# Kernel tuning notes

Hardware: AMD Instinct MI355X
Metric: run time of the kernel (lower is better)

Reference implementation:

```python
import jax, jax.numpy as jnp
from jax import lax
import numpy as np
import math

NUM_CLASSES = 81
N_PER_IMG = 1024
NUM_IMAGES = 8
SCORE_THRESH = 0.05
NMS_THRESH = 0.5
DETS_PER_IMG = 100
WX, WY, WW, WH = 10.0, 10.0, 5.0, 5.0
BBOX_XFORM_CLIP = math.log(1000.0 / 16.0)


def setup_inputs() -> dict:
    key = jax.random.key(0)
    k1, k2, k3, k4 = jax.random.split(key, 4)
    M = NUM_IMAGES * N_PER_IMG
    H, W = 800, 1333
    class_logits = jax.random.normal(k1, (M, NUM_CLASSES), dtype=jnp.float32) * 3.0
    box_regression = jax.random.normal(k2, (M, 4 * NUM_CLASSES), dtype=jnp.float32) * 0.5
    # valid xyxy proposals inside the image
    xy1 = jax.random.uniform(k3, (M, 2), dtype=jnp.float32) * jnp.array([W * 0.7, H * 0.7], jnp.float32)
    wh = jax.random.uniform(k4, (M, 2), dtype=jnp.float32) * jnp.array([W * 0.3, H * 0.3], jnp.float32) + 4.0
    proposals = jnp.concatenate([xy1, xy1 + wh], axis=1)
    return {"class_logits": class_logits, "box_regression": box_regression,
            "proposals": proposals, "height": H, "width": W}


def _decode(rel_codes, boxes):
    widths = boxes[:, 2] - boxes[:, 0] + 1.0
    heights = boxes[:, 3] - boxes[:, 1] + 1.0
    ctr_x = boxes[:, 0] + 0.5 * widths
    ctr_y = boxes[:, 1] + 0.5 * heights
    rel = rel_codes.reshape(rel_codes.shape[0], -1, 4)  # [M, C, 4]
    dx = rel[:, :, 0] / WX
    dy = rel[:, :, 1] / WY
    dw = jnp.minimum(rel[:, :, 2] / WW, BBOX_XFORM_CLIP)
    dh = jnp.minimum(rel[:, :, 3] / WH, BBOX_XFORM_CLIP)
    pctr_x = dx * widths[:, None] + ctr_x[:, None]
    pctr_y = dy * heights[:, None] + ctr_y[:, None]
    pw = jnp.exp(dw) * widths[:, None]
    ph = jnp.exp(dh) * heights[:, None]
    return jnp.stack([pctr_x - 0.5 * pw, pctr_y - 0.5 * ph,
                      pctr_x + 0.5 * pw - 1.0, pctr_y + 0.5 * ph - 1.0], axis=-1)


def _clip(boxes, height, width):
    # boxes [..., 4] xyxy, clamp to [0, W-1] x [0, H-1]
    x = jnp.clip(boxes[..., 0::2], 0.0, float(width - 1))
    y = jnp.clip(boxes[..., 1::2], 0.0, float(height - 1))
    return jnp.stack([x[..., 0], y[..., 0], x[..., 1], y[..., 1]], axis=-1)


def _iou_matrix(b):
    x1, y1, x2, y2 = b[:, 0], b[:, 1], b[:, 2], b[:, 3]
    area = (x2 - x1 + 1.0) * (y2 - y1 + 1.0)
    xx1 = jnp.maximum(x1[:, None], x1[None, :])
    yy1 = jnp.maximum(y1[:, None], y1[None, :])
    xx2 = jnp.minimum(x2[:, None], x2[None, :])
    yy2 = jnp.minimum(y2[:, None], y2[None, :])
    inter = jnp.clip(xx2 - xx1 + 1.0, 0.0) * jnp.clip(yy2 - yy1 + 1.0, 0.0)
    return inter / (area[:, None] + area[None, :] - inter)


def _per_class(scores_j, boxes_j):
    # scores_j [N], boxes_j [N,4] -> sorted scores/boxes + greedy-NMS keep mask
    N = scores_j.shape[0]
    valid = scores_j > SCORE_THRESH
    s = jnp.where(valid, scores_j, 0.0)  # softmax scores are > 0
    order = jnp.argsort(-s)
    s_sorted = s[order]
    b_sorted = boxes_j[order]
    valid_sorted = valid[order]
    iou = _iou_matrix(b_sorted)  # [N, N]
    idxs = jnp.arange(N)

    def body(i, keep):
        sup = (iou[i] > NMS_THRESH) & keep[i] & (idxs > i)
        return keep & ~sup

    keep = lax.fori_loop(0, N, body, valid_sorted)
    return s_sorted, b_sorted, keep


def _per_image(prob_i, boxes_i):
    # prob_i [N, C], boxes_i [N, C, 4]; skip background class 0
    C = prob_i.shape[1]
    fg_scores = prob_i[:, 1:].T                      # [C-1, N]
    fg_boxes = jnp.swapaxes(boxes_i[:, 1:, :], 0, 1)  # [C-1, N, 4]
    s_sorted, b_sorted, keep = jax.vmap(_per_class)(fg_scores, fg_boxes)
    labels = jnp.broadcast_to(jnp.arange(1, C, dtype=jnp.int32)[:, None], s_sorted.shape)
    flat_s = jnp.where(keep, s_sorted, 0.0).reshape(-1)
    vals, idx = lax.top_k(flat_s, DETS_PER_IMG)      # detections-per-image limit
    boxes_out = b_sorted.reshape(-1, 4)[idx]
    labels_out = labels.reshape(-1)[idx]
    ok = vals > SCORE_THRESH
    return (jnp.where(ok, vals, 0.0),
            jnp.where(ok[:, None], boxes_out, 0.0),
            jnp.where(ok, labels_out, 0))


def reference(class_logits, box_regression, proposals, height, width):
    prob = jax.nn.softmax(class_logits, axis=-1)          # [M, C]
    dec = _decode(box_regression, proposals)              # [M, C, 4]
    dec = _clip(dec, height, width)
    B, N, C = NUM_IMAGES, N_PER_IMG, NUM_CLASSES
    prob = prob.reshape(B, N, C)
    dec = dec.reshape(B, N, C, 4)
    scores, boxes, labels = lax.map(lambda a: _per_image(a[0], a[1]), (prob, dec))
    return scores, boxes, labels
```

## Files before the change

### kernel.cpp

```cpp
#include <hip/hip_runtime.h>
#include <stdint.h>
#include <math.h>

#define NCLS 81
#define NFG  80
#define NPI  1024
#define NIMG 8
#define DETS 100
#define SCORE_T 0.05f
#define NMS_T   0.5f
#define NCAND   (NFG * DETS)
#define CAND_CAP 1024
#define FASTN 256
#define ROWS 64

static constexpr float BBOX_CLIP = 4.1351665567423557f;

__global__ __launch_bounds__(256) void softmax_probT(
    const float* __restrict__ logits, float* __restrict__ probT, int M)
{
    __shared__ float tile[ROWS * NCLS];
    __shared__ float mx[ROWS], dn[ROWS];
    int t = threadIdx.x;
    int rbase = blockIdx.x * ROWS;
    for (int idx = t; idx < ROWS * NCLS; idx += 256)
        tile[idx] = logits[(size_t)rbase * NCLS + idx];
    __syncthreads();
    if (t < ROWS) {
        const float* r = tile + t * NCLS;
        float m = r[0];
        #pragma unroll
        for (int j = 1; j < NCLS; ++j) m = fmaxf(m, r[j]);
        float s = 0.f;
        #pragma unroll
        for (int j = 0; j < NCLS; ++j) s += expf(r[j] - m);
        mx[t] = m; dn[t] = s;
    }
    __syncthreads();
    for (int o = t; o < ROWS * NFG; o += 256) {
        int r = o & 63;
        int c = o >> 6;
        probT[(size_t)c * M + rbase + r] = expf(tile[r * NCLS + (c + 1)] - mx[r]) / dn[r];
    }
}

struct ShP2 {
    float box[NPI][4];
    unsigned long long key[NPI];
    unsigned long long skey[NPI];
    int keep[NPI];
    float sbox[FASTN][4];
    float sarea[FASTN];
    unsigned long long mask[FASTN][FASTN/64];
    unsigned long long keepw[FASTN/64];
    unsigned wpre[4];
};

__global__ __launch_bounds__(256) void per_class_nms(
    const float* __restrict__ probT, const float* __restrict__ boxreg,
    const float* __restrict__ props, const int* __restrict__ hptr,
    const int* __restrict__ wptr, int* __restrict__ out_cnt,
    float* __restrict__ out_score, unsigned* __restrict__ out_key,
    float* __restrict__ out_box, int M)
{
    int pid = blockIdx.x;
    int img = pid / NFG;
    int c   = pid % NFG;
    int cls = c + 1;

    __shared__ ShP2 sp;
    __shared__ int cnt;
    int t = threadIdx.x;
    float W1 = (float)(*wptr - 1);
    float H1 = (float)(*hptr - 1);

    if (t == 0) cnt = 0;
    __syncthreads();

    {
        const float4 pv = *(const float4*)(probT + (size_t)c * M + img * NPI + 4 * t);
        float pr[4] = {pv.x, pv.y, pv.z, pv.w};
        #pragma unroll
        for (int j = 0; j < 4; ++j) {
            if (pr[j] > SCORE_T) {
                int m = 4 * t + j;
                int g = img * NPI + m;
                const float4 pb = *(const float4*)(props + (size_t)g * 4);
                float x1 = pb.x, y1 = pb.y, x2 = pb.z, y2 = pb.w;
                float w  = x2 - x1 + 1.0f, h = y2 - y1 + 1.0f;
                float cx = x1 + 0.5f * w,  cy = y1 + 0.5f * h;
                const float4 rc = *(const float4*)(boxreg + (size_t)g * (4 * NCLS) + 4 * cls);
                float dx = rc.x / 10.0f, dy = rc.y / 10.0f;
                float dw = fminf(rc.z / 5.0f, BBOX_CLIP);
                float dh = fminf(rc.w / 5.0f, BBOX_CLIP);
                float pcx = dx * w + cx, pcy = dy * h + cy;
                float pw = expf(dw) * w, ph = expf(dh) * h;
                float bx1 = fminf(fmaxf(pcx - 0.5f * pw, 0.f), W1);
                float by1 = fminf(fmaxf(pcy - 0.5f * ph, 0.f), H1);
                float bx2 = fminf(fmaxf(pcx + 0.5f * pw - 1.0f, 0.f), W1);
                float by2 = fminf(fmaxf(pcy + 0.5f * ph - 1.0f, 0.f), H1);
                sp.box[m][0] = bx1; sp.box[m][1] = by1;
                sp.box[m][2] = bx2; sp.box[m][3] = by2;
                int p = atomicAdd(&cnt, 1);
                sp.key[p] = ((unsigned long long)__float_as_uint(pr[j]) << 32)
                          | (unsigned)(NPI - 1 - m);
            }
        }
    }
    __syncthreads();
    int n = cnt;

    if (n <= 64) {
        if (t < 64) {
            int lane = t;
            unsigned long long k = (lane < n) ? sp.key[lane] : 0ULL;
            #pragma unroll
            for (int kk = 2; kk <= 64; kk <<= 1) {
                #pragma unroll
                for (int j = kk >> 1; j > 0; j >>= 1) {
                    unsigned long long o = __shfl_xor(k, j, 64);
                    bool take_max = (((lane & kk) == 0) == ((lane & j) == 0));
                    k = take_max ? (k > o ? k : o) : (k < o ? k : o);
                }
            }
            bool valid = (lane < n);
            float bx1 = 0.f, by1 = 0.f, bx2 = 0.f, by2 = 0.f, area = 0.f;
            if (valid) {
                int mi = NPI - 1 - (int)(k & 0xFFFFFFFFu);
                bx1 = sp.box[mi][0]; by1 = sp.box[mi][1];
                bx2 = sp.box[mi][2]; by2 = sp.box[mi][3];
                area = (bx2 - bx1 + 1.f) * (by2 - by1 + 1.f);
            }
            unsigned long long sup = 0ULL;
            for (int i = 0; i < n; ++i) {
                bool alive = !((sup >> i) & 1ULL);
                float ax1 = __shfl(bx1, i, 64), ay1 = __shfl(by1, i, 64);
                float ax2 = __shfl(bx2, i, 64), ay2 = __shfl(by2, i, 64);
                float aarea = __shfl(area, i, 64);
                bool s = false;
                if (alive && valid && lane > i) {
                    float xx1 = fmaxf(ax1, bx1), yy1 = fmaxf(ay1, by1);
                    float xx2 = fminf(ax2, bx2), yy2 = fminf(ay2, by2);
                    float iw = fmaxf(xx2 - xx1 + 1.f, 0.f);
                    float ih = fmaxf(yy2 - yy1 + 1.f, 0.f);
                    float inter = iw * ih;
                    s = inter / (aarea + area - inter) > NMS_T;
                }
                sup |= __ballot(s);
            }
            bool kept = valid && !((sup >> lane) & 1ULL);
            unsigned long long keptm = __ballot(kept);
            int rank = __popcll(keptm & ((1ULL << lane) - 1ULL));
            if (kept && rank < DETS) {
                int slot = pid * DETS + rank;
                out_score[slot] = __uint_as_float((unsigned)(k >> 32));
                out_key[slot] = (unsigned)(c * NPI + lane);
                out_box[slot * 4 + 0] = bx1; out_box[slot * 4 + 1] = by1;
                out_box[slot * 4 + 2] = bx2; out_box[slot * 4 + 3] = by2;
            }
            if (lane == 0) {
                int tot = __popcll(keptm);
                out_cnt[pid] = tot < DETS ? tot : DETS;
            }
        }
        return;
    }

    for (int i = t; i < NPI; i += 256) sp.keep[i] = 0;
    for (int i = t; i < n; i += 256) {
        unsigned long long ki = sp.key[i];
        int r = 0;
        for (int j = 0; j < n; ++j) r += (sp.key[j] > ki) ? 1 : 0;
        sp.skey[r] = ki;
    }
    __syncthreads();

    if (n <= FASTN) {
        for (int i = t; i < n; i += 256) {
            int mi = NPI - 1 - (int)(sp.skey[i] & 0xFFFFFFFFu);
            float bx1 = sp.box[mi][0], by1 = sp.box[mi][1];
            float bx2 = sp.box[mi][2], by2 = sp.box[mi][3];
            sp.sbox[i][0] = bx1; sp.sbox[i][1] = by1;
            sp.sbox[i][2] = bx2; sp.sbox[i][3] = by2;
            sp.sarea[i] = (bx2 - bx1 + 1.f) * (by2 - by1 + 1.f);
        }
        __syncthreads();
        int nwords = ((n + 63) >> 6);
        for (int w = t; w < n * (FASTN/64); w += 256) {
            int i = w >> 2, wb = w & 3;
            if (wb >= nwords || ((wb + 1) << 6) - 1 <= i) { sp.mask[i][wb] = 0ULL; continue; }
            float ax1 = sp.sbox[i][0], ay1 = sp.sbox[i][1];
            float ax2 = sp.sbox[i][2], ay2 = sp.sbox[i][3];
            float aarea = sp.sarea[i];
            unsigned long long bits = 0ULL;
            int jbase = wb << 6;
            #pragma unroll 4
            for (int b = 0; b < 64; ++b) {
                int j = jbase + b;
                if (j < n && j > i) {
                    float bx1 = sp.sbox[j][0], by1 = sp.sbox[j][1];
                    float bx2 = sp.sbox[j][2], by2 = sp.sbox[j][3];
                    float xx1 = fmaxf(ax1, bx1), yy1 = fmaxf(ay1, by1);
                    float xx2 = fminf(ax2, bx2), yy2 = fminf(ay2, by2);
                    float iw = fmaxf(xx2 - xx1 + 1.f, 0.f);
                    float ih = fmaxf(yy2 - yy1 + 1.f, 0.f);
                    float inter = iw * ih;
                    if (inter / (aarea + sp.sarea[j] - inter) > NMS_T) bits |= (1ULL << b);
                }
            }
            sp.mask[i][wb] = bits;
        }
        __syncthreads();
        if (t < 64) {
            int lane = t;
            unsigned long long kb = 0ULL;
            if (lane < 4) {
                int rem = n - (lane << 6);
                if (rem >= 64) kb = ~0ULL;
                else if (rem > 0) kb = (1ULL << rem) - 1ULL;
            }
            unsigned long long rm = 0ULL;
            for (int i = 0; i < n; ++i) {
                unsigned long long rw = __shfl(rm, i >> 6, 64);
                if (!((rw >> (i & 63)) & 1ULL)) {
                    unsigned long long mrow = (lane < 4) ? sp.mask[i][lane] : 0ULL;
                    rm |= mrow;
                }
            }
            if (lane < 4) sp.keepw[lane] = kb & ~rm;
        }
        __syncthreads();
        for (int i = t; i < n; i += 256)
            sp.keep[i] = (int)((sp.keepw[i >> 6] >> (i & 63)) & 1ULL);
        __syncthreads();
    } else {
        for (int i = t; i < n; i += 256) sp.keep[i] = 1;
        __syncthreads();
        for (int i = 0; i < n; ++i) {
            if (sp.keep[i]) {
                unsigned long long ki = sp.skey[i];
                int mi = NPI - 1 - (int)(ki & 0xFFFFFFFFu);
                float ax1 = sp.box[mi][0], ay1 = sp.box[mi][1];
                float ax2 = sp.box[mi][2], ay2 = sp.box[mi][3];
                float aarea = (ax2 - ax1 + 1.f) * (ay2 - ay1 + 1.f);
                for (int jj = i + 1 + t; jj < n; jj += 256) {
                    if (sp.keep[jj]) {
                        int mj = NPI - 1 - (int)(sp.skey[jj] & 0xFFFFFFFFu);
                        float bx1 = sp.box[mj][0], by1 = sp.box[mj][1];
                        float bx2 = sp.box[mj][2], by2 = sp.box[mj][3];
                        float xx1 = fmaxf(ax1, bx1), yy1 = fmaxf(ay1, by1);
                        float xx2 = fminf(ax2, bx2), yy2 = fminf(ay2, by2);
                        float iw = fmaxf(xx2 - xx1 + 1.f, 0.f);
                        float ih = fmaxf(yy2 - yy1 + 1.f, 0.f);
                        float inter = iw * ih;
                        float barea = (bx2 - bx1 + 1.f) * (by2 - by1 + 1.f);
                        if (inter / (aarea + barea - inter) > NMS_T) sp.keep[jj] = 0;
                    }
                }
            }
            __syncthreads();
        }
    }

    {
        int lane = t & 63, w = t >> 6;
        int k0 = sp.keep[4 * t], k1 = sp.keep[4 * t + 1];
        int k2 = sp.keep[4 * t + 2], k3 = sp.keep[4 * t + 3];
        unsigned s = (unsigned)(k0 + k1 + k2 + k3);
        unsigned v = s;
        #pragma unroll
        for (int off = 1; off < 64; off <<= 1) {
            unsigned u = __shfl_up(v, off, 64);
            v += (lane >= off) ? u : 0u;
        }
        if (lane == 63) sp.wpre[w] = v;
        __syncthreads();
        unsigned woff = 0;
        for (int w2 = 0; w2 < w; ++w2) woff += sp.wpre[w2];
        unsigned r = v + woff - s;
        #pragma unroll
        for (int j = 0; j < 4; ++j) {
            int i = 4 * t + j;
            int kv = (j == 0) ? k0 : (j == 1) ? k1 : (j == 2) ? k2 : k3;
            if (kv && r < DETS) {
                unsigned long long ki = sp.skey[i];
                int mi = NPI - 1 - (int)(ki & 0xFFFFFFFFu);
                int slot = pid * DETS + (int)r;
                out_score[slot] = __uint_as_float((unsigned)(ki >> 32));
                out_key[slot] = (unsigned)(c * NPI + i);
                out_box[slot * 4 + 0] = sp.box[mi][0];
                out_box[slot * 4 + 1] = sp.box[mi][1];
                out_box[slot * 4 + 2] = sp.box[mi][2];
                out_box[slot * 4 + 3] = sp.box[mi][3];
            }
            r += (unsigned)kv;
        }
        __syncthreads();
        if (t == 0) {
            unsigned tot = sp.wpre[0] + sp.wpre[1] + sp.wpre[2] + sp.wpre[3];
            out_cnt[pid] = (int)(tot < DETS ? tot : DETS);
        }
    }
}

__device__ __forceinline__ void suffix_select256(
    unsigned* hist, unsigned* wtot, int K, int* outB, unsigned* outAbove)
{
    int t = threadIdx.x, lane = t & 63, w = t >> 6;
    unsigned loc[16]; unsigned ps = 0;
    #pragma unroll
    for (int j = 0; j < 16; ++j) { loc[j] = hist[t * 16 + j]; ps += loc[j]; }
    unsigned v = ps;
    #pragma unroll
    for (int off = 1; off < 64; off <<= 1) {
        unsigned u = __shfl_down(v, off, 64);
        v += (lane + off < 64) ? u : 0u;
    }
    if (lane == 0) wtot[w] = v;
    __syncthreads();
    unsigned woff = 0;
    for (int w2 = w + 1; w2 < 4; ++w2) woff += wtot[w2];
    unsigned base = v + woff - ps;
    unsigned suf = 0;
    #pragma unroll
    for (int j = 15; j >= 0; --j) {
        unsigned A = base + suf;
        if ((int)A < K && (int)(A + loc[j]) >= K) { *outB = t * 16 + j; *outAbove = A; }
        suf += loc[j];
    }
    __syncthreads();
}

__global__ __launch_bounds__(256) void topk_merge(
    const int* __restrict__ cnts, const float* __restrict__ escore,
    const unsigned* __restrict__ ekey, const float* __restrict__ ebox,
    float* __restrict__ out)
{
    int img = blockIdx.x;
    __shared__ unsigned sc[NCAND];
    __shared__ unsigned hist[4096];
    __shared__ unsigned long long cand[CAND_CAP];
    __shared__ int scnts[NFG];
    __shared__ unsigned wtot[4];
    __shared__ int sB1, sB2, sNc;
    __shared__ unsigned sAb1, sAb2;

    int t = threadIdx.x;
    if (t < NFG) scnts[t] = cnts[img * NFG + t];
    if (t == 0) { sB1 = 0; sB2 = 0; sNc = 0; sAb1 = 0; sAb2 = 0; }
    for (int i = t; i < 4096; i += 256) hist[i] = 0;
    __syncthreads();

    for (int p = t; p < NCAND; p += 256) {
        unsigned fb = 0;
        if ((p % DETS) < scnts[p / DETS]) fb = __float_as_uint(escore[img * NCAND + p]);
        sc[p] = fb;
        if (fb) atomicAdd(&hist[fb >> 19], 1u);
    }
    __syncthreads();
    suffix_select256(hist, wtot, DETS, &sB1, &sAb1);
    int B1 = sB1; unsigned ab1 = sAb1;

    for (int i = t; i < 4096; i += 256) hist[i] = 0;
    __syncthreads();
    for (int p = t; p < NCAND; p += 256) {
        unsigned fb = sc[p];
        if (fb && (int)(fb >> 19) == B1) atomicAdd(&hist[(fb >> 7) & 0xFFFu], 1u);
    }
    __syncthreads();
    suffix_select256(hist, wtot, DETS - (int)ab1, &sB2, &sAb2);
    int B2 = sB2;

    for (int p = t; p < NCAND; p += 256) {
        unsigned fb = sc[p];
        if (fb) {
            int d1 = (int)(fb >> 19);
            bool ok = d1 > B1 || (d1 == B1 && (int)((fb >> 7) & 0xFFFu) >= B2);
            if (ok) {
                int pos = atomicAdd(&sNc, 1);
                if (pos < CAND_CAP) {
                    unsigned fk = ekey[img * NCAND + p];
                    cand[pos] = ((unsigned long long)fb << 32)
                              | (((0x1FFFFu - fk) << 13) | (unsigned)p);
                }
            }
        }
    }
    __syncthreads();
    int nc = sNc < CAND_CAP ? sNc : CAND_CAP;

    float* oScore = out;
    float* oBox   = out + NIMG * DETS;
    float* oLab   = out + NIMG * DETS * 5;

    for (int k = t; k < DETS; k += 256) {
        if (k >= nc) {
            int o = img * DETS + k;
            oScore[o] = 0.f;
            oBox[o * 4 + 0] = 0.f; oBox[o * 4 + 1] = 0.f;
            oBox[o * 4 + 2] = 0.f; oBox[o * 4 + 3] = 0.f;
            oLab[o] = 0.f;
        }
    }

    for (int i = t; i < nc; i += 256) {
        unsigned long long ki = cand[i];
        int r = 0;
        for (int j = 0; j < nc; ++j) r += (cand[j] > ki) ? 1 : 0;
        if (r < DETS) {
            float scv = __uint_as_float((unsigned)(ki >> 32));
            unsigned low = (unsigned)(ki & 0xFFFFFFFFu);
            unsigned flatkey = 0x1FFFFu - ((low >> 13) & 0x1FFFFu);
            int p = (int)(low & 0x1FFFu);
            int gp = img * NCAND + p;
            int o = img * DETS + r;
            oScore[o] = scv;
            oBox[o * 4 + 0] = ebox[gp * 4 + 0];
            oBox[o * 4 + 1] = ebox[gp * 4 + 1];
            oBox[o * 4 + 2] = ebox[gp * 4 + 2];
            oBox[o * 4 + 3] = ebox[gp * 4 + 3];
            oLab[o] = (float)((flatkey >> 10) + 1);
        }
    }
}

extern "C" void kernel_launch(void* const* d_in, const int* in_sizes, int n_in,
                              void* d_out, int out_size, void* d_ws, size_t ws_size,
                              hipStream_t stream) {
    const float* logits = (const float*)d_in[0];
    const float* boxreg = (const float*)d_in[1];
    const float* props  = (const float*)d_in[2];
    const int*   hptr   = (const int*)d_in[3];
    const int*   wptr   = (const int*)d_in[4];
    float* out = (float*)d_out;
    int M = in_sizes[0] / NCLS;

    char* ws = (char*)d_ws;
    float*    probT  = (float*)ws;    ws += (size_t)NFG * M * sizeof(float);
    int*      gcnt   = (int*)ws;      ws += (size_t)NIMG * NFG * sizeof(int);
    float*    escore = (float*)ws;    ws += (size_t)NIMG * NCAND * sizeof(float);
    unsigned* ekey   = (unsigned*)ws; ws += (size_t)NIMG * NCAND * sizeof(unsigned);
    float*    ebox   = (float*)ws;    ws += (size_t)NIMG * NCAND * 4 * sizeof(float);

    softmax_probT<<<M / ROWS, 256, 0, stream>>>(logits, probT, M);
    per_class_nms<<<NIMG * NFG, 256, 0, stream>>>(
        probT, boxreg, props, hptr, wptr, gcnt, escore, ekey, ebox, M);
    topk_merge<<<NIMG, 256, 0, stream>>>(gcnt, escore, ekey, ebox, out);
}
```

Before: 66.43 us.

## Rewrite per-class NMS as single-wavefront chunked greedy suppression

The per-class NMS kernel now runs one 64-lane wavefront per (image, class) instead of 256 threads. Candidate compaction uses ballot/popcount in place of shared atomics, and the candidate's compacted position is packed into the sort key. The bitmask matrix and serial fallback paths are replaced by a chunked greedy NMS that broadcasts boxes with readlane and keeps a suppression word per 64-box chunk. This cuts shared-memory footprint and block-level syncs, but the O(n^2) rank sort and per-class work now run on a quarter of the threads, and the number of blocks is unchanged.

```diff
diff --git a/kernel.cpp b/kernel.cpp
--- a/kernel.cpp
+++ b/kernel.cpp
@@ -11,10 +11,17 @@
 #define NMS_T   0.5f
 #define NCAND   (NFG * DETS)
 #define CAND_CAP 1024
-#define FASTN 256
 #define ROWS 64
 
 static constexpr float BBOX_CLIP = 4.1351665567423557f;
+
+__device__ __forceinline__ float rlf(float v, int i) {
+#if __has_builtin(__builtin_amdgcn_readlane)
+    return __uint_as_float((unsigned)__builtin_amdgcn_readlane((int)__float_as_uint(v), i));
+#else
+    return __shfl(v, i, 64);
+#endif
+}
 
 __global__ __launch_bounds__(256) void softmax_probT(
     const float* __restrict__ logits, float* __restrict__ probT, int M)
@@ -44,19 +51,7 @@
     }
 }
 
-struct ShP2 {
-    float box[NPI][4];
-    unsigned long long key[NPI];
-    unsigned long long skey[NPI];
-    int keep[NPI];
-    float sbox[FASTN][4];
-    float sarea[FASTN];
-    unsigned long long mask[FASTN][FASTN/64];
-    unsigned long long keepw[FASTN/64];
-    unsigned wpre[4];
-};
-
-__global__ __launch_bounds__(256) void per_class_nms(
+__global__ __launch_bounds__(64) void per_class_nms(
     const float* __restrict__ probT, const float* __restrict__ boxreg,
     const float* __restrict__ props, const int* __restrict__ hptr,
     const int* __restrict__ wptr, int* __restrict__ out_cnt,
@@ -67,24 +62,31 @@
     int img = pid / NFG;
     int c   = pid % NFG;
     int cls = c + 1;
-
-    __shared__ ShP2 sp;
-    __shared__ int cnt;
-    int t = threadIdx.x;
+    int lane = threadIdx.x;
+
+    __shared__ unsigned long long pkey[NPI];
+    __shared__ unsigned long long skey[NPI];
+    __shared__ float pbox[NPI][4];
+    __shared__ unsigned long long remv[16];
+
     float W1 = (float)(*wptr - 1);
     float H1 = (float)(*hptr - 1);
 
-    if (t == 0) cnt = 0;
-    __syncthreads();
-
-    {
-        const float4 pv = *(const float4*)(probT + (size_t)c * M + img * NPI + 4 * t);
+    int cnt = 0;
+    const float* pT = probT + (size_t)c * M + img * NPI;
+
+    #pragma unroll
+    for (int it = 0; it < NPI / 256; ++it) {
+        float4 pv = *(const float4*)(pT + it * 256 + lane * 4);
         float pr[4] = {pv.x, pv.y, pv.z, pv.w};
         #pragma unroll
         for (int j = 0; j < 4; ++j) {
-            if (pr[j] > SCORE_T) {
-                int m = 4 * t + j;
+            bool pass = pr[j] > SCORE_T;
+            unsigned long long bal = __ballot(pass);
+            if (pass) {
+                int m = it * 256 + lane * 4 + j;
                 int g = img * NPI + m;
+                int mypos = cnt + __popcll(bal & ((1ULL << lane) - 1ULL));
                 const float4 pb = *(const float4*)(props + (size_t)g * 4);
                 float x1 = pb.x, y1 = pb.y, x2 = pb.z, y2 = pb.w;
                 float w  = x2 - x1 + 1.0f, h = y2 - y1 + 1.0f;
@@ -99,207 +101,173 @@
                 float by1 = fminf(fmaxf(pcy - 0.5f * ph, 0.f), H1);
                 float bx2 = fminf(fmaxf(pcx + 0.5f * pw - 1.0f, 0.f), W1);
                 float by2 = fminf(fmaxf(pcy + 0.5f * ph - 1.0f, 0.f), H1);
-                sp.box[m][0] = bx1; sp.box[m][1] = by1;
-                sp.box[m][2] = bx2; sp.box[m][3] = by2;
-                int p = atomicAdd(&cnt, 1);
-                sp.key[p] = ((unsigned long long)__float_as_uint(pr[j]) << 32)
-                          | (unsigned)(NPI - 1 - m);
-            }
-        }
-    }
-    __syncthreads();
+                pbox[mypos][0] = bx1; pbox[mypos][1] = by1;
+                pbox[mypos][2] = bx2; pbox[mypos][3] = by2;
+                pkey[mypos] = ((unsigned long long)__float_as_uint(pr[j]) << 32)
+                            | ((unsigned)(NPI - 1 - m) << 10) | (unsigned)mypos;
+            }
+            cnt += __popcll(bal);
+        }
+    }
     int n = cnt;
+    __syncthreads();
 
     if (n <= 64) {
-        if (t < 64) {
-            int lane = t;
-            unsigned long long k = (lane < n) ? sp.key[lane] : 0ULL;
+        unsigned long long k = (lane < n) ? pkey[lane] : 0ULL;
+        #pragma unroll
+        for (int kk = 2; kk <= 64; kk <<= 1) {
             #pragma unroll
-            for (int kk = 2; kk <= 64; kk <<= 1) {
-                #pragma unroll
-                for (int j = kk >> 1; j > 0; j >>= 1) {
-                    unsigned long long o = __shfl_xor(k, j, 64);
-                    bool take_max = (((lane & kk) == 0) == ((lane & j) == 0));
-                    k = take_max ? (k > o ? k : o) : (k < o ? k : o);
-                }
-            }
-            bool valid = (lane < n);
-            float bx1 = 0.f, by1 = 0.f, bx2 = 0.f, by2 = 0.f, area = 0.f;
-            if (valid) {
-                int mi = NPI - 1 - (int)(k & 0xFFFFFFFFu);
-                bx1 = sp.box[mi][0]; by1 = sp.box[mi][1];
-                bx2 = sp.box[mi][2]; by2 = sp.box[mi][3];
-                area = (bx2 - bx1 + 1.f) * (by2 - by1 + 1.f);
-            }
-            unsigned long long sup = 0ULL;
-            for (int i = 0; i < n; ++i) {
-                bool alive = !((sup >> i) & 1ULL);
-                float ax1 = __shfl(bx1, i, 64), ay1 = __shfl(by1, i, 64);
-                float ax2 = __shfl(bx2, i, 64), ay2 = __shfl(by2, i, 64);
-                float aarea = __shfl(area, i, 64);
+            for (int j = kk >> 1; j > 0; j >>= 1) {
+                unsigned long long o = __shfl_xor(k, j, 64);
+                bool take_max = (((lane & kk) == 0) == ((lane & j) == 0));
+                k = take_max ? (k > o ? k : o) : (k < o ? k : o);
+            }
+        }
+        bool valid = (lane < n);
+        float bx1 = 0.f, by1 = 0.f, bx2 = 0.f, by2 = 0.f, area = 0.f;
+        if (valid) {
+            int pos = (int)(k & 0x3FFu);
+            bx1 = pbox[pos][0]; by1 = pbox[pos][1];
+            bx2 = pbox[pos][2]; by2 = pbox[pos][3];
+            area = (bx2 - bx1 + 1.f) * (by2 - by1 + 1.f);
+        }
+        unsigned long long sup = 0ULL;
+        for (int i = 0; i < n; ++i) {
+            if ((sup >> i) & 1ULL) continue;
+            float ax1 = rlf(bx1, i), ay1 = rlf(by1, i);
+            float ax2 = rlf(bx2, i), ay2 = rlf(by2, i);
+            float aarea = rlf(area, i);
+            bool s = false;
+            if (valid && lane > i) {
+                float xx1 = fmaxf(ax1, bx1), yy1 = fmaxf(ay1, by1);
+                float xx2 = fminf(ax2, bx2), yy2 = fminf(ay2, by2);
+                float iw = fmaxf(xx2 - xx1 + 1.f, 0.f);
+                float ih = fmaxf(yy2 - yy1 + 1.f, 0.f);
+                float inter = iw * ih;
+                s = inter / (aarea + area - inter) > NMS_T;
+            }
+            sup |= __ballot(s);
+        }
+        bool kept = valid && !((sup >> lane) & 1ULL);
+        unsigned long long keptm = __ballot(kept);
+        int rank = __popcll(keptm & ((1ULL << lane) - 1ULL));
+        if (kept && rank < DETS) {
+            int slot = pid * DETS + rank;
+            out_score[slot] = __uint_as_float((unsigned)(k >> 32));
+            out_key[slot] = (unsigned)(c * NPI + lane);
+            out_box[slot * 4 + 0] = bx1; out_box[slot * 4 + 1] = by1;
+            out_box[slot * 4 + 2] = bx2; out_box[slot * 4 + 3] = by2;
+        }
+        if (lane == 0) {
+            int tot = __popcll(keptm);
+            out_cnt[pid] = tot < DETS ? tot : DETS;
+        }
+        return;
+    }
+
+    for (int i = lane; i < n; i += 64) {
+        unsigned long long ki = pkey[i];
+        int r = 0;
+        for (int j = 0; j < n; ++j) r += (pkey[j] > ki) ? 1 : 0;
+        skey[r] = ki;
+    }
+    if (lane < 16) remv[lane] = 0ULL;
+    __syncthreads();
+
+    int nch = (n + 63) >> 6;
+    for (int a = 0; a < nch; ++a) {
+        int ea = a * 64 + lane;
+        bool va = ea < n;
+        float bx1 = 0.f, by1 = 0.f, bx2 = 0.f, by2 = 0.f, area = 0.f;
+        if (va) {
+            int pos = (int)(skey[ea] & 0x3FFu);
+            bx1 = pbox[pos][0]; by1 = pbox[pos][1];
+            bx2 = pbox[pos][2]; by2 = pbox[pos][3];
+            area = (bx2 - bx1 + 1.f) * (by2 - by1 + 1.f);
+        }
+        unsigned long long sup = remv[a];
+        int lim = (n - a * 64 < 64) ? (n - a * 64) : 64;
+        for (int i = 0; i < lim; ++i) {
+            if ((sup >> i) & 1ULL) continue;
+            float ax1 = rlf(bx1, i), ay1 = rlf(by1, i);
+            float ax2 = rlf(bx2, i), ay2 = rlf(by2, i);
+            float aarea = rlf(area, i);
+            bool s = false;
+            if (va && lane > i) {
+                float xx1 = fmaxf(ax1, bx1), yy1 = fmaxf(ay1, by1);
+                float xx2 = fminf(ax2, bx2), yy2 = fminf(ay2, by2);
+                float iw = fmaxf(xx2 - xx1 + 1.f, 0.f);
+                float ih = fmaxf(yy2 - yy1 + 1.f, 0.f);
+                float inter = iw * ih;
+                s = inter / (aarea + area - inter) > NMS_T;
+            }
+            sup |= __ballot(s);
+        }
+        if (lane == 0) remv[a] = sup;
+        for (int b = a + 1; b < nch; ++b) {
+            int eb = b * 64 + lane;
+            bool vb = eb < n;
+            float cx1 = 0.f, cy1 = 0.f, cx2 = 0.f, cy2 = 0.f, carea = 0.f;
+            if (vb) {
+                int pos = (int)(skey[eb] & 0x3FFu);
+                cx1 = pbox[pos][0]; cy1 = pbox[pos][1];
+                cx2 = pbox[pos][2]; cy2 = pbox[pos][3];
+                carea = (cx2 - cx1 + 1.f) * (cy2 - cy1 + 1.f);
+            }
+            unsigned long long supb = 0ULL;
+            for (int i = 0; i < lim; ++i) {
+                if ((sup >> i) & 1ULL) continue;
+                float ax1 = rlf(bx1, i), ay1 = rlf(by1, i);
+                float ax2 = rlf(bx2, i), ay2 = rlf(by2, i);
+                float aarea = rlf(area, i);
                 bool s = false;
-                if (alive && valid && lane > i) {
-                    float xx1 = fmaxf(ax1, bx1), yy1 = fmaxf(ay1, by1);
-                    float xx2 = fminf(ax2, bx2), yy2 = fminf(ay2, by2);
+                if (vb) {
+                    float xx1 = fmaxf(ax1, cx1), yy1 = fmaxf(ay1, cy1);
+                    float xx2 = fminf(ax2, cx2), yy2 = fminf(ay2, cy2);
                     float iw = fmaxf(xx2 - xx1 + 1.f, 0.f);
                     float ih = fmaxf(yy2 - yy1 + 1.f, 0.f);
                     float inter = iw * ih;
-                    s = inter / (aarea + area - inter) > NMS_T;
+                    s = inter / (aarea + carea - inter) > NMS_T;
                 }
-                sup |= __ballot(s);
-            }
-            bool kept = valid && !((sup >> lane) & 1ULL);
-            unsigned long long keptm = __ballot(kept);
-            int rank = __popcll(keptm & ((1ULL << lane) - 1ULL));
-            if (kept && rank < DETS) {
-                int slot = pid * DETS + rank;
-                out_score[slot] = __uint_as_float((unsigned)(k >> 32));
-                out_key[slot] = (unsigned)(c * NPI + lane);
-                out_box[slot * 4 + 0] = bx1; out_box[slot * 4 + 1] = by1;
-                out_box[slot * 4 + 2] = bx2; out_box[slot * 4 + 3] = by2;
-            }
-            if (lane == 0) {
-                int tot = __popcll(keptm);
-                out_cnt[pid] = tot < DETS ? tot : DETS;
-            }
-        }
-        return;
-    }
-
-    for (int i = t; i < NPI; i += 256) sp.keep[i] = 0;
-    for (int i = t; i < n; i += 256) {
-        unsigned long long ki = sp.key[i];
-        int r = 0;
-        for (int j = 0; j < n; ++j) r += (sp.key[j] > ki) ? 1 : 0;
-        sp.skey[r] = ki;
-    }
-    __syncthreads();
-
-    if (n <= FASTN) {
-        for (int i = t; i < n; i += 256) {
-            int mi = NPI - 1 - (int)(sp.skey[i] & 0xFFFFFFFFu);
-            float bx1 = sp.box[mi][0], by1 = sp.box[mi][1];
-            float bx2 = sp.box[mi][2], by2 = sp.box[mi][3];
-            sp.sbox[i][0] = bx1; sp.sbox[i][1] = by1;
-            sp.sbox[i][2] = bx2; sp.sbox[i][3] = by2;
-            sp.sarea[i] = (bx2 - bx1 + 1.f) * (by2 - by1 + 1.f);
+                supb |= __ballot(s);
+            }
+            if (lane == 0) remv[b] |= supb;
+            __syncthreads();
         }
         __syncthreads();
-        int nwords = ((n + 63) >> 6);
-        for (int w = t; w < n * (FASTN/64); w += 256) {
-            int i = w >> 2, wb = w & 3;
-            if (wb >= nwords || ((wb + 1) << 6) - 1 <= i) { sp.mask[i][wb] = 0ULL; continue; }
-            float ax1 = sp.sbox[i][0], ay1 = sp.sbox[i][1];
-            float ax2 = sp.sbox[i][2], ay2 = sp.sbox[i][3];
-            float aarea = sp.sarea[i];
-            unsigned long long bits = 0ULL;
-            int jbase = wb << 6;
-            #pragma unroll 4
-            for (int b = 0; b < 64; ++b) {
-                int j = jbase + b;
-                if (j < n && j > i) {
-                    float bx1 = sp.sbox[j][0], by1 = sp.sbox[j][1];
-                    float bx2 = sp.sbox[j][2], by2 = sp.sbox[j][3];
-                    float xx1 = fmaxf(ax1, bx1), yy1 = fmaxf(ay1, by1);
-                    float xx2 = fminf(ax2, bx2), yy2 = fminf(ay2, by2);
-                    float iw = fmaxf(xx2 - xx1 + 1.f, 0.f);
-                    float ih = fmaxf(yy2 - yy1 + 1.f, 0.f);
-                    float inter = iw * ih;
-                    if (inter / (aarea + sp.sarea[j] - inter) > NMS_T) bits |= (1ULL << b);
-                }
-            }
-            sp.mask[i][wb] = bits;
-        }
-        __syncthreads();
-        if (t < 64) {
-            int lane = t;
-            unsigned long long kb = 0ULL;
-            if (lane < 4) {
-                int rem = n - (lane << 6);
-                if (rem >= 64) kb = ~0ULL;
-                else if (rem > 0) kb = (1ULL << rem) - 1ULL;
-            }
-            unsigned long long rm = 0ULL;
-            for (int i = 0; i < n; ++i) {
-                unsigned long long rw = __shfl(rm, i >> 6, 64);
-                if (!((rw >> (i & 63)) & 1ULL)) {
-                    unsigned long long mrow = (lane < 4) ? sp.mask[i][lane] : 0ULL;
-                    rm |= mrow;
-                }
-            }
-            if (lane < 4) sp.keepw[lane] = kb & ~rm;
-        }
-        __syncthreads();
-        for (int i = t; i < n; i += 256)
-            sp.keep[i] = (int)((sp.keepw[i >> 6] >> (i & 63)) & 1ULL);
-        __syncthreads();
-    } else {
-        for (int i = t; i < n; i += 256) sp.keep[i] = 1;
-        __syncthreads();
-        for (int i = 0; i < n; ++i) {
-            if (sp.keep[i]) {
-                unsigned long long ki = sp.skey[i];
-                int mi = NPI - 1 - (int)(ki & 0xFFFFFFFFu);
-                float ax1 = sp.box[mi][0], ay1 = sp.box[mi][1];
-                float ax2 = sp.box[mi][2], ay2 = sp.box[mi][3];
-                float aarea = (ax2 - ax1 + 1.f) * (ay2 - ay1 + 1.f);
-                for (int jj = i + 1 + t; jj < n; jj += 256) {
-                    if (sp.keep[jj]) {
-                        int mj = NPI - 1 - (int)(sp.skey[jj] & 0xFFFFFFFFu);
-                        float bx1 = sp.box[mj][0], by1 = sp.box[mj][1];
-                        float bx2 = sp.box[mj][2], by2 = sp.box[mj][3];
-                        float xx1 = fmaxf(ax1, bx1), yy1 = fmaxf(ay1, by1);
-                        float xx2 = fminf(ax2, bx2), yy2 = fminf(ay2, by2);
-                        float iw = fmaxf(xx2 - xx1 + 1.f, 0.f);
-                        float ih = fmaxf(yy2 - yy1 + 1.f, 0.f);
-                        float inter = iw * ih;
-                        float barea = (bx2 - bx1 + 1.f) * (by2 - by1 + 1.f);
-                        if (inter / (aarea + barea - inter) > NMS_T) sp.keep[jj] = 0;
-                    }
-                }
-            }
-            __syncthreads();
-        }
-    }
-
-    {
-        int lane = t & 63, w = t >> 6;
-        int k0 = sp.keep[4 * t], k1 = sp.keep[4 * t + 1];
-        int k2 = sp.keep[4 * t + 2], k3 = sp.keep[4 * t + 3];
-        unsigned s = (unsigned)(k0 + k1 + k2 + k3);
-        unsigned v = s;
-        #pragma unroll
-        for (int off = 1; off < 64; off <<= 1) {
-            unsigned u = __shfl_up(v, off, 64);
-            v += (lane >= off) ? u : 0u;
-        }
-        if (lane == 63) sp.wpre[w] = v;
-        __syncthreads();
-        unsigned woff = 0;
-        for (int w2 = 0; w2 < w; ++w2) woff += sp.wpre[w2];
-        unsigned r = v + woff - s;
-        #pragma unroll
-        for (int j = 0; j < 4; ++j) {
-            int i = 4 * t + j;
-            int kv = (j == 0) ? k0 : (j == 1) ? k1 : (j == 2) ? k2 : k3;
-            if (kv && r < DETS) {
-                unsigned long long ki = sp.skey[i];
-                int mi = NPI - 1 - (int)(ki & 0xFFFFFFFFu);
-                int slot = pid * DETS + (int)r;
+    }
+
+    unsigned long long vmasks[16];
+    int base[17];
+    base[0] = 0;
+    for (int ch = 0; ch < nch; ++ch) {
+        int rem = n - ch * 64;
+        unsigned long long vm = (rem >= 64) ? ~0ULL : ((1ULL << rem) - 1ULL);
+        vmasks[ch] = vm;
+        base[ch + 1] = base[ch] + __popcll(~remv[ch] & vm);
+    }
+    for (int e = lane; e < n; e += 64) {
+        int ch = e >> 6;
+        unsigned long long rm = remv[ch];
+        bool kept = !((rm >> (e & 63)) & 1ULL);
+        if (kept) {
+            int r = base[ch] + __popcll(~rm & vmasks[ch] & ((1ULL << (e & 63)) - 1ULL));
+            if (r < DETS) {
+                unsigned long long ki = skey[e];
+                int pos = (int)(ki & 0x3FFu);
+                int slot = pid * DETS + r;
                 out_score[slot] = __uint_as_float((unsigned)(ki >> 32));
-                out_key[slot] = (unsigned)(c * NPI + i);
-                out_box[slot * 4 + 0] = sp.box[mi][0];
-                out_box[slot * 4 + 1] = sp.box[mi][1];
-                out_box[slot * 4 + 2] = sp.box[mi][2];
-                out_box[slot * 4 + 3] = sp.box[mi][3];
-            }
-            r += (unsigned)kv;
-        }
-        __syncthreads();
-        if (t == 0) {
-            unsigned tot = sp.wpre[0] + sp.wpre[1] + sp.wpre[2] + sp.wpre[3];
-            out_cnt[pid] = (int)(tot < DETS ? tot : DETS);
-        }
+                out_key[slot] = (unsigned)(c * NPI + e);
+                out_box[slot * 4 + 0] = pbox[pos][0];
+                out_box[slot * 4 + 1] = pbox[pos][1];
+                out_box[slot * 4 + 2] = pbox[pos][2];
+                out_box[slot * 4 + 3] = pbox[pos][3];
+            }
+        }
+    }
+    if (lane == 0) {
+        int tot = base[nch];
+        out_cnt[pid] = tot < DETS ? tot : DETS;
     }
 }
 
@@ -443,7 +411,7 @@
     float*    ebox   = (float*)ws;    ws += (size_t)NIMG * NCAND * 4 * sizeof(float);
 
     softmax_probT<<<M / ROWS, 256, 0, stream>>>(logits, probT, M);
-    per_class_nms<<<NIMG * NFG, 256, 0, stream>>>(
+    per_class_nms<<<NIMG * NFG, 64, 0, stream>>>(
         probT, boxreg, props, hptr, wptr, gcnt, escore, ekey, ebox, M);
     topk_merge<<<NIMG, 256, 0, stream>>>(gcnt, escore, ekey, ebox, out);
 }
```

Result: slower. 71.74 us (+8.0%).
